# Performance work log

Hardware: AMD Instinct MI355X
Metric: run time of the kernel (lower is better)

## Reference

```python
import jax, jax.numpy as jnp
import numpy as np

N_NODES = 100000
N_EDGES = 1600000
IN_DIM = 512
HID_DIM = 64


def gcn_conv(x, src, dst, ew, W, b, n_nodes):
    """PyG-style GCNConv: add self-loops, symmetric norm, transform-then-propagate."""
    loop = jnp.arange(n_nodes)
    src_sl = jnp.concatenate([src, loop])
    dst_sl = jnp.concatenate([dst, loop])
    ew_sl = jnp.concatenate([ew, jnp.ones((n_nodes,), ew.dtype)])  # self-loop weight 1
    # degree at target nodes (weighted)
    deg = jax.ops.segment_sum(ew_sl, dst_sl, num_segments=n_nodes)
    dinv = jnp.where(deg > 0, jax.lax.rsqrt(deg), 0.0)
    norm = dinv[src_sl] * ew_sl * dinv[dst_sl]          # [E+N]
    h = x @ W                                           # [N, out] transform first
    msg = h[src_sl] * norm[:, None]                     # gather + scale
    out = jax.ops.segment_sum(msg, dst_sl, num_segments=n_nodes)  # scatter-add
    return out + b


def setup_inputs() -> dict:
    key = jax.random.key(0)
    k = jax.random.split(key, 8)
    x = jax.random.normal(k[0], (N_NODES, IN_DIM), dtype=jnp.float32)
    edge_index = jax.random.randint(k[1], (2, N_EDGES), 0, N_NODES, dtype=jnp.int64)
    edge_weight = jax.random.uniform(k[2], (N_EDGES,), dtype=jnp.float32)
    # Glorot-ish init for layer weights, zeros bias (PyG default)
    W1 = jax.random.normal(k[3], (IN_DIM, HID_DIM), dtype=jnp.float32) / np.sqrt(IN_DIM)
    b1 = jnp.zeros((HID_DIM,), dtype=jnp.float32)
    W2 = jax.random.normal(k[4], (HID_DIM, HID_DIM), dtype=jnp.float32) / np.sqrt(HID_DIM)
    b2 = jnp.zeros((HID_DIM,), dtype=jnp.float32)
    return {"x": x, "edge_index": edge_index, "edge_weight": edge_weight,
            "W1": W1, "b1": b1, "W2": W2, "b2": b2}


def reference(x, edge_index, edge_weight, W1, b1, W2, b2):
    src, dst = edge_index[0], edge_index[1]
    h = gcn_conv(x, src, dst, edge_weight, W1, b1, N_NODES)
    h = jax.nn.relu(h)
    out = gcn_conv(h, src, dst, edge_weight, W2, b2, N_NODES)
    return out
```

## Files before the change

### kernel.cpp

```cpp
#include <hip/hip_runtime.h>

#define N_NODES 100000
#define N_EDGES 1600000
#define IN_DIM 512
#define HID 64
#define CAP 48


__global__ __launch_bounds__(256) void k_zero_cnt(int* __restrict__ cnt) {
  int i = blockIdx.x * 256 + threadIdx.x;
  if (i < N_NODES) cnt[i] = 0;
}

__global__ __launch_bounds__(256) void k_bucket(const int* __restrict__ dst,
                                                int* __restrict__ cnt,
                                                int* __restrict__ bucket) {
  int e = blockIdx.x * 256 + threadIdx.x;
  if (e < N_EDGES) {
    int dd = dst[e];
    int p = atomicAdd(&cnt[dd], 1);
    if (p < CAP) bucket[(size_t)dd * CAP + p] = e;
  }
}

__global__ __launch_bounds__(256) void k_dinv_b(const int* __restrict__ cnt,
                                                const int* __restrict__ bucket,
                                                const float* __restrict__ ew,
                                                float* __restrict__ dinv) {
  const int t = threadIdx.x;
  const int node = blockIdx.x * 4 + (t >> 6);
  if (node >= N_NODES) return;
  const int lane = t & 63;
  const int cv = min(cnt[node], CAP);
  float w = 0.f;
  if (lane < cv) w = ew[bucket[(size_t)node * CAP + lane]];
#pragma unroll
  for (int off = 32; off; off >>= 1) w += __shfl_xor(w, off, 64);
  if (lane == 0) dinv[node] = rsqrtf(1.0f + w);
}


template <int K, bool RELU>
__global__ __launch_bounds__(256) void k_gemm(const float* __restrict__ X,
                                              const float* __restrict__ W,
                                              float* __restrict__ H) {
  __shared__ float xs[64][68];
  __shared__ float ws[64][64];
  const int t = threadIdx.x;
  const int row0 = blockIdx.x * 64;
  const int tc = t & 15;
  const int tr = t >> 4;
  const int kq = t & 15;
  const int rs = t >> 4;

  float acc[4][4] = {};

  for (int k0 = 0; k0 < K; k0 += 64) {
#pragma unroll
    for (int i = 0; i < 4; ++i) {
      int row = rs + 16 * i;
      float4 v = make_float4(0.f, 0.f, 0.f, 0.f);
      if (row0 + row < N_NODES)
        v = *reinterpret_cast<const float4*>(
            &X[(size_t)(row0 + row) * K + k0 + kq * 4]);
      if (RELU) {
        v.x = fmaxf(v.x, 0.f); v.y = fmaxf(v.y, 0.f);
        v.z = fmaxf(v.z, 0.f); v.w = fmaxf(v.w, 0.f);
      }
      *reinterpret_cast<float4*>(&xs[row][kq * 4]) = v;
    }
#pragma unroll
    for (int i = 0; i < 4; ++i) {
      int k = rs + 16 * i;
      float4 v = *reinterpret_cast<const float4*>(
          &W[(size_t)(k0 + k) * HID + kq * 4]);
      *reinterpret_cast<float4*>(&ws[k][kq * 4]) = v;
    }
    __syncthreads();

#pragma unroll
    for (int kk = 0; kk < 64; kk += 4) {
      float4 xv[4], wv[4];
#pragma unroll
      for (int i = 0; i < 4; ++i)
        xv[i] = *reinterpret_cast<const float4*>(&xs[tr * 4 + i][kk]);
#pragma unroll
      for (int j = 0; j < 4; ++j)
        wv[j] = *reinterpret_cast<const float4*>(&ws[kk + j][tc * 4]);
#pragma unroll
      for (int i = 0; i < 4; ++i) {
        const float xr[4] = {xv[i].x, xv[i].y, xv[i].z, xv[i].w};
#pragma unroll
        for (int j = 0; j < 4; ++j) {
          acc[i][0] += xr[j] * wv[j].x;
          acc[i][1] += xr[j] * wv[j].y;
          acc[i][2] += xr[j] * wv[j].z;
          acc[i][3] += xr[j] * wv[j].w;
        }
      }
    }
    __syncthreads();
  }

#pragma unroll
  for (int i = 0; i < 4; ++i) {
    int row = row0 + tr * 4 + i;
    if (row < N_NODES) {
      float4 v = make_float4(acc[i][0], acc[i][1], acc[i][2], acc[i][3]);
      *reinterpret_cast<float4*>(&H[(size_t)row * HID + tc * 4]) = v;
    }
  }
}

__global__ __launch_bounds__(256) void k_agg_b(const float* __restrict__ h,
                                               const int* __restrict__ cnt,
                                               const int* __restrict__ bucket,
                                               const int* __restrict__ src,
                                               const float* __restrict__ ew,
                                               const float* __restrict__ dinv,
                                               const float* __restrict__ b,
                                               float* __restrict__ out) {
  const int t = threadIdx.x;
  const int node = blockIdx.x * 4 + (t >> 6);
  if (node >= N_NODES) return;
  const int d = t & 63;
  const int cv = min(cnt[node], CAP);
  const float dn = dinv[node];

  int s_l = 0;
  float c_l = 0.f;
  if (d < cv) {
    int e = bucket[(size_t)node * CAP + d];
    s_l = src[e];
    c_l = ew[e] * dinv[s_l];
  }

  float acc = h[(size_t)node * HID + d] * dn;
  int i = 0;
  for (; i + 4 <= cv; i += 4) {
    int s0 = __shfl(s_l, i, 64), s1 = __shfl(s_l, i + 1, 64);
    int s2 = __shfl(s_l, i + 2, 64), s3 = __shfl(s_l, i + 3, 64);
    float c0 = __shfl(c_l, i, 64), c1 = __shfl(c_l, i + 1, 64);
    float c2 = __shfl(c_l, i + 2, 64), c3 = __shfl(c_l, i + 3, 64);
    float h0 = h[(size_t)s0 * HID + d];
    float h1 = h[(size_t)s1 * HID + d];
    float h2 = h[(size_t)s2 * HID + d];
    float h3 = h[(size_t)s3 * HID + d];
    acc += c0 * h0 + c1 * h1 + c2 * h2 + c3 * h3;
  }
  for (; i < cv; ++i) {
    int s = __shfl(s_l, i, 64);
    float c = __shfl(c_l, i, 64);
    acc += c * h[(size_t)s * HID + d];
  }
  out[(size_t)node * HID + d] = dn * acc + b[d];
}


extern "C" void kernel_launch(void* const* d_in, const int* in_sizes, int n_in,
                              void* d_out, int out_size, void* d_ws, size_t ws_size,
                              hipStream_t stream) {
  const float* x  = (const float*)d_in[0];
  const int*   ei = (const int*)d_in[1];
  const float* ew = (const float*)d_in[2];
  const float* W1 = (const float*)d_in[3];
  const float* b1 = (const float*)d_in[4];
  const float* W2 = (const float*)d_in[5];
  const float* b2 = (const float*)d_in[6];
  const int* src = ei;
  const int* dst = ei + N_EDGES;
  float* out = (float*)d_out;

  int*   bucket = (int*)d_ws;
  float* hbuf   = (float*)(bucket + (size_t)N_NODES * CAP);
  int*   cnt    = (int*)(hbuf + (size_t)N_NODES * HID);
  float* dinv   = (float*)(cnt + N_NODES);

  dim3 b256(256);
  const int gN = (N_NODES + 255) / 256;
  const int gE = (N_EDGES + 255) / 256;
  const int gW = (N_NODES + 3) / 4;

  k_zero_cnt<<<gN, b256, 0, stream>>>(cnt);
  k_bucket<<<gE, b256, 0, stream>>>(dst, cnt, bucket);
  k_dinv_b<<<gW, b256, 0, stream>>>(cnt, bucket, ew, dinv);

  k_gemm<IN_DIM, false><<<(N_NODES + 63) / 64, b256, 0, stream>>>(x, W1, hbuf);
  k_agg_b<<<gW, b256, 0, stream>>>(hbuf, cnt, bucket, src, ew, dinv, b1, out);

  k_gemm<HID, true><<<(N_NODES + 63) / 64, b256, 0, stream>>>(out, W2, hbuf);
  k_agg_b<<<gW, b256, 0, stream>>>(hbuf, cnt, bucket, src, ew, dinv, b2, out);
}
```

Baseline: 746.0 us.

## Replace FP32 SIMT GEMMs with bf16 MFMA kernels using pre-swizzled weights

```diff
diff --git a/kernel.cpp b/kernel.cpp
--- a/kernel.cpp
+++ b/kernel.cpp
@@ -5,6 +5,25 @@
 #define IN_DIM 512
 #define HID 64
 #define CAP 48
+
+typedef __attribute__((ext_vector_type(8))) short bf16x8;
+typedef __attribute__((ext_vector_type(4))) float f32x4;
+
+__device__ inline unsigned short f2bf(float f) {
+  union { float f; unsigned u; } v;
+  v.f = f;
+  unsigned r = v.u + 0x7fff + ((v.u >> 16) & 1);
+  return (unsigned short)(r >> 16);
+}
+
+__device__ inline bf16x8 cvt8(float4 a, float4 b) {
+  bf16x8 r;
+  r[0] = (short)f2bf(a.x); r[1] = (short)f2bf(a.y);
+  r[2] = (short)f2bf(a.z); r[3] = (short)f2bf(a.w);
+  r[4] = (short)f2bf(b.x); r[5] = (short)f2bf(b.y);
+  r[6] = (short)f2bf(b.z); r[7] = (short)f2bf(b.w);
+  return r;
+}
 
 
 __global__ __launch_bounds__(256) void k_zero_cnt(int* __restrict__ cnt) {
@@ -39,77 +58,67 @@
   if (lane == 0) dinv[node] = rsqrtf(1.0f + w);
 }
 
-
 template <int K, bool RELU>
-__global__ __launch_bounds__(256) void k_gemm(const float* __restrict__ X,
-                                              const float* __restrict__ W,
-                                              float* __restrict__ H) {
-  __shared__ float xs[64][68];
-  __shared__ float ws[64][64];
+__global__ __launch_bounds__(256) void k_gemm_mfma(const float* __restrict__ X,
+                                                   const float* __restrict__ Wm,
+                                                   float* __restrict__ H) {
+  __shared__ unsigned short wlds[K * HID];
   const int t = threadIdx.x;
-  const int row0 = blockIdx.x * 64;
-  const int tc = t & 15;
-  const int tr = t >> 4;
-  const int kq = t & 15;
-  const int rs = t >> 4;
-
-  float acc[4][4] = {};
-
-  for (int k0 = 0; k0 < K; k0 += 64) {
-#pragma unroll
-    for (int i = 0; i < 4; ++i) {
-      int row = rs + 16 * i;
-      float4 v = make_float4(0.f, 0.f, 0.f, 0.f);
-      if (row0 + row < N_NODES)
-        v = *reinterpret_cast<const float4*>(
-            &X[(size_t)(row0 + row) * K + k0 + kq * 4]);
-      if (RELU) {
-        v.x = fmaxf(v.x, 0.f); v.y = fmaxf(v.y, 0.f);
-        v.z = fmaxf(v.z, 0.f); v.w = fmaxf(v.w, 0.f);
-      }
-      *reinterpret_cast<float4*>(&xs[row][kq * 4]) = v;
-    }
-#pragma unroll
-    for (int i = 0; i < 4; ++i) {
-      int k = rs + 16 * i;
-      float4 v = *reinterpret_cast<const float4*>(
-          &W[(size_t)(k0 + k) * HID + kq * 4]);
-      *reinterpret_cast<float4*>(&ws[k][kq * 4]) = v;
-    }
-    __syncthreads();
-
-#pragma unroll
-    for (int kk = 0; kk < 64; kk += 4) {
-      float4 xv[4], wv[4];
-#pragma unroll
-      for (int i = 0; i < 4; ++i)
-        xv[i] = *reinterpret_cast<const float4*>(&xs[tr * 4 + i][kk]);
-#pragma unroll
-      for (int j = 0; j < 4; ++j)
-        wv[j] = *reinterpret_cast<const float4*>(&ws[kk + j][tc * 4]);
-#pragma unroll
-      for (int i = 0; i < 4; ++i) {
-        const float xr[4] = {xv[i].x, xv[i].y, xv[i].z, xv[i].w};
-#pragma unroll
-        for (int j = 0; j < 4; ++j) {
-          acc[i][0] += xr[j] * wv[j].x;
-          acc[i][1] += xr[j] * wv[j].y;
-          acc[i][2] += xr[j] * wv[j].z;
-          acc[i][3] += xr[j] * wv[j].w;
-        }
-      }
-    }
-    __syncthreads();
-  }
-
-#pragma unroll
-  for (int i = 0; i < 4; ++i) {
-    int row = row0 + tr * 4 + i;
-    if (row < N_NODES) {
-      float4 v = make_float4(acc[i][0], acc[i][1], acc[i][2], acc[i][3]);
-      *reinterpret_cast<float4*>(&H[(size_t)row * HID + tc * 4]) = v;
-    }
-  }
+
+  for (int idx = t; idx < K * HID / 4; idx += 256) {
+    float4 wv = *reinterpret_cast<const float4*>(&Wm[idx * 4]);
+    int k = (idx * 4) >> 6, n0 = (idx * 4) & 63;
+    float wf[4] = {wv.x, wv.y, wv.z, wv.w};
+#pragma unroll
+    for (int q = 0; q < 4; ++q) {
+      int n = n0 + q;
+      int g = k >> 5, kc = (k & 31) >> 3, j = k & 7;
+      int off = ((((g * 4 + (n >> 4)) * 4 + kc) * 16 + (n & 15)) << 3) | j;
+      wlds[off] = f2bf(wf[q]);
+    }
+  }
+  __syncthreads();
+
+  const int wave = t >> 6, lane = t & 63;
+  const int l15 = lane & 15, kc = lane >> 4;
+  const int arow = blockIdx.x * 64 + wave * 16 + l15;
+  const bool avalid = arow < N_NODES;
+  const float* xrow = X + (size_t)arow * K;
+
+  f32x4 acc[4] = {};
+
+#pragma unroll 4
+  for (int g = 0; g < K / 32; ++g) {
+    float4 a0 = make_float4(0.f, 0.f, 0.f, 0.f);
+    float4 a1 = make_float4(0.f, 0.f, 0.f, 0.f);
+    if (avalid) {
+      a0 = *reinterpret_cast<const float4*>(xrow + g * 32 + kc * 8);
+      a1 = *reinterpret_cast<const float4*>(xrow + g * 32 + kc * 8 + 4);
+    }
+    if (RELU) {
+      a0.x = fmaxf(a0.x, 0.f); a0.y = fmaxf(a0.y, 0.f);
+      a0.z = fmaxf(a0.z, 0.f); a0.w = fmaxf(a0.w, 0.f);
+      a1.x = fmaxf(a1.x, 0.f); a1.y = fmaxf(a1.y, 0.f);
+      a1.z = fmaxf(a1.z, 0.f); a1.w = fmaxf(a1.w, 0.f);
+    }
+    bf16x8 af = cvt8(a0, a1);
+    const unsigned short* wb = &wlds[(((g * 16 + kc) * 16 + l15)) << 3];
+#pragma unroll
+    for (int nt = 0; nt < 4; ++nt) {
+      bf16x8 bfr = *reinterpret_cast<const bf16x8*>(wb + nt * 512);
+      acc[nt] = __builtin_amdgcn_mfma_f32_16x16x32_bf16(af, bfr, acc[nt], 0, 0, 0);
+    }
+  }
+
+  const int crow0 = blockIdx.x * 64 + wave * 16 + kc * 4;
+#pragma unroll
+  for (int nt = 0; nt < 4; ++nt)
+#pragma unroll
+    for (int r = 0; r < 4; ++r) {
+      int crow = crow0 + r;
+      if (crow < N_NODES)
+        H[(size_t)crow * HID + nt * 16 + l15] = acc[nt][r];
+    }
 }
 
 __global__ __launch_bounds__(256) void k_agg_b(const float* __restrict__ h,
@@ -180,14 +189,15 @@
   const int gN = (N_NODES + 255) / 256;
   const int gE = (N_EDGES + 255) / 256;
   const int gW = (N_NODES + 3) / 4;
+  const int gG = (N_NODES + 63) / 64;
 
   k_zero_cnt<<<gN, b256, 0, stream>>>(cnt);
   k_bucket<<<gE, b256, 0, stream>>>(dst, cnt, bucket);
   k_dinv_b<<<gW, b256, 0, stream>>>(cnt, bucket, ew, dinv);
 
-  k_gemm<IN_DIM, false><<<(N_NODES + 63) / 64, b256, 0, stream>>>(x, W1, hbuf);
+  k_gemm_mfma<IN_DIM, false><<<gG, b256, 0, stream>>>(x, W1, hbuf);
   k_agg_b<<<gW, b256, 0, stream>>>(hbuf, cnt, bucket, src, ew, dinv, b1, out);
 
-  k_gemm<HID, true><<<(N_NODES + 63) / 64, b256, 0, stream>>>(out, W2, hbuf);
+  k_gemm_mfma<HID, true><<<gG, b256, 0, stream>>>(out, W2, hbuf);
   k_agg_b<<<gW, b256, 0, stream>>>(hbuf, cnt, bucket, src, ew, dinv, b2, out);
 }
```

New measurement: 726.8 us. -2.6%, faster.
